# Kernel tuning notes

Hardware: AMD Instinct MI355X
Metric: run time of the kernel (lower is better)

## Reference

```python
import jax, jax.numpy as jnp
import numpy as np

D = 768
NH = 12
HD = D // NH
N_MLP = 3072
LN_EPS = 1e-6


def layer_norm(x, g, b, eps=LN_EPS):
    mu = jnp.mean(x, axis=-1, keepdims=True)
    var = jnp.mean(jnp.square(x - mu), axis=-1, keepdims=True)
    return (x - mu) * jax.lax.rsqrt(var + eps) * g + b


def setup_inputs() -> dict:
    key = jax.random.key(0)
    ks = jax.random.split(key, 6)
    x = jax.random.normal(ks[0], (2, 4096, D), dtype=jnp.float32)
    # torch Linear weights are (out, in); init std=0.02, zero bias
    W_qkv = 0.02 * jax.random.normal(ks[1], (3 * D, D), dtype=jnp.float32)
    b_qkv = jnp.zeros((3 * D,), dtype=jnp.float32)
    W_proj = 0.02 * jax.random.normal(ks[2], (D, D), dtype=jnp.float32)
    b_proj = jnp.zeros((D,), dtype=jnp.float32)
    W1 = 0.02 * jax.random.normal(ks[3], (N_MLP, D), dtype=jnp.float32)
    b1 = jnp.zeros((N_MLP,), dtype=jnp.float32)
    W2 = 0.02 * jax.random.normal(ks[4], (D, N_MLP), dtype=jnp.float32)
    b2 = jnp.zeros((D,), dtype=jnp.float32)
    g1 = jnp.ones((D,), dtype=jnp.float32)
    beta1 = jnp.zeros((D,), dtype=jnp.float32)
    g2 = jnp.ones((D,), dtype=jnp.float32)
    beta2 = jnp.zeros((D,), dtype=jnp.float32)
    return dict(x=x, W_qkv=W_qkv, b_qkv=b_qkv, W_proj=W_proj, b_proj=b_proj,
                W1=W1, b1=b1, W2=W2, b2=b2,
                g1=g1, beta1=beta1, g2=g2, beta2=beta2)


def reference(x, W_qkv, b_qkv, W_proj, b_proj, W1, b1, W2, b2, g1, beta1, g2, beta2):
    B, T, d = x.shape
    scale = HD ** (-0.5)
    # --- attention branch (pre-norm) ---
    h = layer_norm(x, g1, beta1)
    qkv = h @ W_qkv.T + b_qkv                      # [B,T,3d]
    qkv = qkv.reshape(B, T, 3, NH, HD)
    q, k, v = qkv[:, :, 0], qkv[:, :, 1], qkv[:, :, 2]  # [B,T,NH,HD]
    logits = jnp.einsum('bthc,bshc->bhts', q, k) * scale
    attn = jax.nn.softmax(logits, axis=-1)
    out = jnp.einsum('bhts,bshc->bthc', attn, v).reshape(B, T, d)
    out = out @ W_proj.T + b_proj
    x = x + out
    # --- MLP branch (pre-norm) ---
    h = layer_norm(x, g2, beta2)
    h = jax.nn.gelu(h @ W1.T + b1, approximate=False)
    h = h @ W2.T + b2
    return x + h
```

## Files before the change

kernel.cpp:

```cpp
#include <hip/hip_runtime.h>
#include <cmath>

typedef __attribute__((ext_vector_type(4))) float f32x4;
typedef __attribute__((ext_vector_type(16))) float f32x16;
typedef __attribute__((ext_vector_type(8))) __bf16 bf16x8;
typedef __attribute__((ext_vector_type(8))) unsigned short u16x8;
typedef __attribute__((ext_vector_type(4))) unsigned short u16x4;
typedef __attribute__((ext_vector_type(2))) unsigned int u32x2;
typedef __attribute__((ext_vector_type(4))) unsigned int u32x4;

#define DEV __device__ __forceinline__

DEV unsigned short f2b(float v) {
  __bf16 b = (__bf16)v;
  return __builtin_bit_cast(unsigned short, b);
}

DEV unsigned int cvtpk(float lo, float hi) {
  unsigned int r;
  asm("v_cvt_pk_bf16_f32 %0, %1, %2" : "=v"(r) : "v"(lo), "v"(hi));
  return r;
}

DEV float exp2a(float x) {
  float r;
  asm("v_exp_f32 %0, %1" : "=v"(r) : "v"(x));
  return r;
}

DEV void swap32(unsigned int& x, unsigned int& y) {
  asm("v_permlane32_swap_b32 %0, %1" : "+v"(x), "+v"(y));
}

DEV u32x2 tr_b16(const unsigned short* p) {
  u32x2 r;
  asm volatile("ds_read_b64_tr_b16 %0, %1"
               : "=v"(r)
               : "v"((unsigned int)(unsigned long long)p)
               : "memory");
  return r;
}

DEV void gll16(const void* g, const void* l) {
  __builtin_amdgcn_global_load_lds(
      (const __attribute__((address_space(1))) unsigned int*)(unsigned long long)g,
      (__attribute__((address_space(3))) unsigned int*)(unsigned int)(unsigned long long)l,
      16, 0, 0);
}

__global__ void k_cvt_bf16(const float* __restrict__ src,
                           unsigned short* __restrict__ dst, int n4) {
  int i = blockIdx.x * blockDim.x + threadIdx.x;
  if (i >= n4) return;
  float4 v = ((const float4*)src)[i];
  u16x4 o = {f2b(v.x), f2b(v.y), f2b(v.z), f2b(v.w)};
  *(u16x4*)(dst + (size_t)i * 4) = o;
}

__global__ void k_ln(const float* __restrict__ x, const float* __restrict__ g,
                     const float* __restrict__ be, unsigned short* __restrict__ out) {
  int row = blockIdx.x;
  int l = threadIdx.x;
  const float* xr = x + (size_t)row * 768;
  float4 v[3];
  float s = 0.f, sq = 0.f;
#pragma unroll
  for (int j = 0; j < 3; ++j) {
    v[j] = ((const float4*)xr)[l + 64 * j];
    s += v[j].x + v[j].y + v[j].z + v[j].w;
    sq += v[j].x * v[j].x + v[j].y * v[j].y + v[j].z * v[j].z + v[j].w * v[j].w;
  }
#pragma unroll
  for (int m = 1; m < 64; m <<= 1) {
    s += __shfl_xor(s, m);
    sq += __shfl_xor(sq, m);
  }
  float mu = s * (1.f / 768.f);
  float var = sq * (1.f / 768.f) - mu * mu;
  float rs = rsqrtf(var + 1e-6f);
  unsigned short* orow = out + (size_t)row * 768;
#pragma unroll
  for (int j = 0; j < 3; ++j) {
    int c4 = l + 64 * j;
    float4 gv = ((const float4*)g)[c4];
    float4 bv = ((const float4*)be)[c4];
    u16x4 o = {f2b((v[j].x - mu) * rs * gv.x + bv.x),
               f2b((v[j].y - mu) * rs * gv.y + bv.y),
               f2b((v[j].z - mu) * rs * gv.z + bv.z),
               f2b((v[j].w - mu) * rs * gv.w + bv.w)};
    *(u16x4*)(orow + c4 * 4) = o;
  }
}

template <int MODE, int BM>
__global__ __launch_bounds__(256, 2) void k_gemm(
    const unsigned short* __restrict__ A, const unsigned short* __restrict__ Bw,
    const float* __restrict__ bias, const float* __restrict__ res,
    void* __restrict__ outp, int N, int K) {
  __shared__ unsigned short As[3][BM * 32];
  __shared__ unsigned short Bs[3][128 * 32];
  constexpr int MR = BM / 32;
  constexpr int AI = BM / 64;
  constexpr int LPT = AI + 2;
  const int tid = threadIdx.x;
  const int w = tid >> 6, l = tid & 63;
  const int wr = w >> 1, wc = w & 1;
  const int lr = l & 15, lg = l >> 4;
  const int nwg = gridDim.x * gridDim.y;
  const int bid = blockIdx.y * gridDim.x + blockIdx.x;
  const int swz = (bid & 7) * (nwg >> 3) + (bid >> 3);
  const int bx = swz % gridDim.x, by = swz / gridDim.x;
  const int brow = by * BM, bcol = bx * 128;

  auto stage = [&](int buf, int kt) {
#pragma unroll
    for (int i = 0; i < AI; ++i) {
      int c = i * 256 + tid;
      int row = c >> 2, cg = (c & 3) ^ (row & 3);
      gll16(A + (size_t)(brow + row) * K + kt + cg * 8,
            (const char*)&As[buf][0] + (i * 256 + (w << 6)) * 16);
    }
#pragma unroll
    for (int i = 0; i < 2; ++i) {
      int c = i * 256 + tid;
      int row = c >> 2, cg = (c & 3) ^ (row & 3);
      gll16(Bw + (size_t)(bcol + row) * K + kt + cg * 8,
            (const char*)&Bs[buf][0] + (i * 256 + (w << 6)) * 16);
    }
  };

  stage(0, 0);
  if (32 < K) stage(1, 32);
  f32x4 acc[MR][4] = {};
  int cur = 0, nxt2 = 2;
  for (int kt = 0; kt < K; kt += 32) {
    if (kt + 32 < K) {
      if constexpr (LPT == 4)
        asm volatile("s_waitcnt vmcnt(4)" ::: "memory");
      else
        asm volatile("s_waitcnt vmcnt(3)" ::: "memory");
    } else {
      asm volatile("s_waitcnt vmcnt(0)" ::: "memory");
    }
    __builtin_amdgcn_s_barrier();
    __builtin_amdgcn_sched_barrier(0);
    if (kt + 64 < K) {
      stage(nxt2, kt + 64);
      nxt2 = (nxt2 == 2) ? 0 : nxt2 + 1;
    }
    bf16x8 af[MR], bfr[4];
#pragma unroll
    for (int m = 0; m < MR; ++m) {
      int row = wr * (BM / 2) + m * 16 + lr;
      af[m] = *(const bf16x8*)&As[cur][row * 32 + ((lg ^ (row & 3)) << 3)];
    }
#pragma unroll
    for (int n = 0; n < 4; ++n) {
      int row = wc * 64 + n * 16 + lr;
      bfr[n] = *(const bf16x8*)&Bs[cur][row * 32 + ((lg ^ (row & 3)) << 3)];
    }
#pragma unroll
    for (int m = 0; m < MR; ++m)
#pragma unroll
      for (int n = 0; n < 4; ++n)
        acc[m][n] = __builtin_amdgcn_mfma_f32_16x16x32_bf16(af[m], bfr[n], acc[m][n], 0, 0, 0);
    cur = (cur == 2) ? 0 : cur + 1;
  }
#pragma unroll
  for (int n = 0; n < 4; ++n) {
    int col = bcol + wc * 64 + n * 16 + lr;
    float bv = bias[col];
#pragma unroll
    for (int m = 0; m < MR; ++m) {
      int row0 = brow + wr * (BM / 2) + m * 16 + lg * 4;
#pragma unroll
      for (int r = 0; r < 4; ++r) {
        size_t idx = (size_t)(row0 + r) * N + col;
        float v = acc[m][n][r] + bv;
        if (MODE == 0) {
          ((unsigned short*)outp)[idx] = f2b(v);
        } else if (MODE == 1) {
          ((float*)outp)[idx] = v + res[idx];
        } else if (MODE == 2) {
          ((unsigned short*)outp)[idx] = f2b(0.5f * v * (1.f + erff(v * 0.70710678f)));
        } else {
          ((float*)outp)[idx] = v + res[idx];
        }
      }
    }
  }
}

__global__ __launch_bounds__(256, 4) void k_attn(const unsigned short* __restrict__ qkv,
                                                 f32x4* __restrict__ Opart,
                                                 float* __restrict__ ml) {
  __shared__ unsigned short Ks[2][64 * 64];
  __shared__ unsigned short Vs[2][4 * 64 * 16];
  const int tid = threadIdx.x;
  const int w = tid >> 6, l = tid & 63;
  const int lq = l & 31, hi = l >> 5;
  const int p = blockIdx.x;
  const int linear = (p & 7) * 192 + (p >> 3);
  const int bh = linear >> 6, rem = linear & 63;
  const int qt = rem >> 1, half = rem & 1;
  const int b = bh / 12, h = bh % 12;
  const size_t base = (size_t)b * 4096 * 2304;
  const int qbase = qt * 128 + w * 32;
  const int kv0 = half * 2048;

  const float SC = 0.18033688f;
  bf16x8 qb[4];
#pragma unroll
  for (int s = 0; s < 4; ++s) {
    u16x8 raw = *(const u16x8*)(qkv + base + (size_t)(qbase + lq) * 2304 + h * 64 +
                                s * 16 + hi * 8);
    u32x4 pk;
#pragma unroll
    for (int d = 0; d < 4; ++d) {
      float f0 = __builtin_bit_cast(float, (unsigned int)raw[2 * d] << 16) * SC;
      float f1 = __builtin_bit_cast(float, (unsigned int)raw[2 * d + 1] << 16) * SC;
      pk[d] = cvtpk(f0, f1);
    }
    qb[s] = __builtin_bit_cast(bf16x8, pk);
  }

  const unsigned short* pK = qkv + base + (size_t)(kv0 + 16 * w + (l >> 3)) * 2304 + 768 +
                             h * 64 + (((l & 7) ^ ((l >> 3) & 7)) << 3);
  const unsigned short* pV = qkv + base + (size_t)(kv0 + (l >> 1)) * 2304 + 1536 + h * 64 +
                             w * 16 + ((l & 1) << 3);
  const size_t STEP = (size_t)64 * 2304;

  {
    const char* dK = (const char*)&Ks[0][0] + w * 2048;
    const char* dV = (const char*)&Vs[0][0] + w * 2048;
    gll16(pK, dK);
    gll16(pK + 8 * 2304, dK + 1024);
    gll16(pV, dV);
    gll16(pV + 32 * 2304, dV + 1024);
    pK += STEP;
    pV += STEP;
  }

  f32x16 O[2] = {};
  float lrun = 0.f;

  int it = 0;
  for (int t = 0; t < 32; ++t, it ^= 1) {
    asm volatile("s_waitcnt vmcnt(0)" ::: "memory");
    __syncthreads();
    if (t < 31) {
      const char* dK = (const char*)&Ks[it ^ 1][0] + w * 2048;
      const char* dV = (const char*)&Vs[it ^ 1][0] + w * 2048;
      gll16(pK, dK);
      gll16(pK + 8 * 2304, dK + 1024);
      gll16(pV, dV);
      gll16(pV + 32 * 2304, dV + 1024);
      pK += STEP;
      pV += STEP;
    }

    f32x16 st[2] = {{0}, {0}};
    __builtin_amdgcn_s_setprio(1);
#pragma unroll
    for (int kt = 0; kt < 2; ++kt) {
      int key = kt * 32 + lq;
#pragma unroll
      for (int s = 0; s < 4; ++s) {
        bf16x8 ka =
            *(const bf16x8*)&Ks[it][key * 64 + ((s * 16 + hi * 8) ^ ((key & 7) << 3))];
        st[kt] = __builtin_amdgcn_mfma_f32_32x32x16_bf16(ka, qb[s], st[kt], 0, 0, 0);
      }
    }
    __builtin_amdgcn_s_setprio(0);

    float s0 = 0.f, s1 = 0.f, s2 = 0.f, s3 = 0.f;
#pragma unroll
    for (int kt = 0; kt < 2; ++kt) {
#pragma unroll
      for (int r = 0; r < 16; r += 4) {
        float p0 = exp2a(st[kt][r + 0]);
        float p1 = exp2a(st[kt][r + 1]);
        float p2 = exp2a(st[kt][r + 2]);
        float p3 = exp2a(st[kt][r + 3]);
        st[kt][r + 0] = p0;
        st[kt][r + 1] = p1;
        st[kt][r + 2] = p2;
        st[kt][r + 3] = p3;
        s0 += p0;
        s1 += p1;
        s2 += p2;
        s3 += p3;
      }
    }
    float ssum = (s0 + s1) + (s2 + s3);
    lrun += ssum + __shfl_xor(ssum, 32);

    u32x4 pf[4];
#pragma unroll
    for (int kt = 0; kt < 2; ++kt)
#pragma unroll
      for (int h2 = 0; h2 < 2; ++h2) {
        int r0 = h2 * 8;
        unsigned int a0 = cvtpk(st[kt][r0 + 0], st[kt][r0 + 1]);
        unsigned int a1 = cvtpk(st[kt][r0 + 2], st[kt][r0 + 3]);
        unsigned int b0 = cvtpk(st[kt][r0 + 4], st[kt][r0 + 5]);
        unsigned int b1 = cvtpk(st[kt][r0 + 6], st[kt][r0 + 7]);
        swap32(a0, b0);
        swap32(a1, b1);
        pf[kt * 2 + h2] = u32x4{a0, a1, b0, b1};
      }

#pragma unroll
    for (int hb = 0; hb < 2; ++hb) {
      u32x2 vt[4][2];
      const unsigned short* vbase = &Vs[it][(hb * 2 + (lq >> 4)) * 1024 + (lq & 15)];
#pragma unroll
      for (int s = 0; s < 4; ++s)
#pragma unroll
        for (int t2 = 0; t2 < 2; ++t2)
          vt[s][t2] = tr_b16(vbase + ((s * 16 + hi * 8 + t2 * 4) << 4));
      asm volatile("s_waitcnt lgkmcnt(0)" ::: "memory");
      __builtin_amdgcn_sched_barrier(0);
      __builtin_amdgcn_s_setprio(1);
#pragma unroll
      for (int s = 0; s < 4; ++s) {
        u32x4 vv = {vt[s][0].x, vt[s][0].y, vt[s][1].x, vt[s][1].y};
        O[hb] = __builtin_amdgcn_mfma_f32_32x32x16_bf16(
            __builtin_bit_cast(bf16x8, vv), __builtin_bit_cast(bf16x8, pf[s]), O[hb], 0, 0, 0);
      }
      __builtin_amdgcn_s_setprio(0);
    }
  }

  if (hi == 0) ml[(linear * 4 + w) * 32 + lq] = lrun;
#pragma unroll
  for (int hb = 0; hb < 2; ++hb)
#pragma unroll
    for (int g = 0; g < 4; ++g) {
      int k = hb * 4 + g;
      f32x4 v = {O[hb][4 * g + 0], O[hb][4 * g + 1], O[hb][4 * g + 2], O[hb][4 * g + 3]};
      Opart[((linear * 4 + w) * 8 + k) * 64 + l] = v;
    }
}

__global__ __launch_bounds__(256) void k_merge(const f32x4* __restrict__ Opart,
                                               const float* __restrict__ ml,
                                               unsigned short* __restrict__ out) {
  const int g = blockIdx.x;
  const int bh = g >> 5, qt = g & 31;
  const int b = bh / 12, h = bh % 12;
  const int tid = threadIdx.x;
  const int w = tid >> 6, l = tid & 63;
  const int lq = l & 31, hi = l >> 5;
  const int bidA = bh * 64 + qt * 2;
  const int bidB = bidA + 1;
  float l0 = ml[(bidA * 4 + w) * 32 + lq];
  float l1 = ml[(bidB * 4 + w) * 32 + lq];
  float rl = 1.f / (l0 + l1);
  const int t = qt * 128 + w * 32 + lq;
  unsigned short* orow = out + (size_t)(b * 4096 + t) * 768 + h * 64;
#pragma unroll
  for (int hb = 0; hb < 2; ++hb)
#pragma unroll
    for (int gg = 0; gg < 4; ++gg) {
      int k = hb * 4 + gg;
      f32x4 va = Opart[((bidA * 4 + w) * 8 + k) * 64 + l];
      f32x4 vb = Opart[((bidB * 4 + w) * 8 + k) * 64 + l];
      f32x4 v = (va + vb) * rl;
      unsigned int d0 = cvtpk(v[0], v[1]);
      unsigned int d1 = cvtpk(v[2], v[3]);
      *(u32x2*)(orow + hb * 32 + 8 * gg + 4 * hi) = u32x2{d0, d1};
    }
}

extern "C" void kernel_launch(void* const* d_in, const int* in_sizes, int n_in,
                              void* d_out, int out_size, void* d_ws, size_t ws_size,
                              hipStream_t stream) {
  const float* x = (const float*)d_in[0];
  const float* Wqkv = (const float*)d_in[1];
  const float* bqkv = (const float*)d_in[2];
  const float* Wproj = (const float*)d_in[3];
  const float* bproj = (const float*)d_in[4];
  const float* W1 = (const float*)d_in[5];
  const float* b1 = (const float*)d_in[6];
  const float* W2 = (const float*)d_in[7];
  const float* b2 = (const float*)d_in[8];
  const float* g1 = (const float*)d_in[9];
  const float* be1 = (const float*)d_in[10];
  const float* g2 = (const float*)d_in[11];
  const float* be2 = (const float*)d_in[12];

  char* ws = (char*)d_ws;
  unsigned short* wqkv = (unsigned short*)(ws + 0);
  unsigned short* wproj = (unsigned short*)(ws + 3538944);
  unsigned short* ww1 = (unsigned short*)(ws + 4718592);
  unsigned short* ww2 = (unsigned short*)(ws + 9437184);
  unsigned short* h1 = (unsigned short*)(ws + 14155776);
  unsigned short* qkvb = (unsigned short*)(ws + 26738688);
  unsigned short* attno = (unsigned short*)(ws + 64487424);
  float* x1 = (float*)(ws + 77070336);
  unsigned short* h2 = (unsigned short*)(ws + 102236160);
  unsigned short* m1 = (unsigned short*)(ws + 114819072);
  f32x4* Opart = (f32x4*)m1;
  float* mlbuf = (float*)h1;

  k_cvt_bf16<<<1728, 256, 0, stream>>>(Wqkv, wqkv, 442368);
  k_cvt_bf16<<<576, 256, 0, stream>>>(Wproj, wproj, 147456);
  k_cvt_bf16<<<2304, 256, 0, stream>>>(W1, ww1, 589824);
  k_cvt_bf16<<<2304, 256, 0, stream>>>(W2, ww2, 589824);

  k_ln<<<8192, 64, 0, stream>>>(x, g1, be1, h1);
  k_gemm<0, 128><<<dim3(18, 64), 256, 0, stream>>>(h1, wqkv, bqkv, nullptr, qkvb, 2304, 768);
  k_attn<<<1536, 256, 0, stream>>>(qkvb, Opart, mlbuf);
  k_merge<<<768, 256, 0, stream>>>(Opart, mlbuf, attno);
  k_gemm<1, 64><<<dim3(6, 128), 256, 0, stream>>>(attno, wproj, bproj, x, x1, 768, 768);
  k_ln<<<8192, 64, 0, stream>>>(x1, g2, be2, h2);
  k_gemm<2, 128><<<dim3(24, 64), 256, 0, stream>>>(h2, ww1, b1, nullptr, m1, 3072, 768);
  k_gemm<3, 64><<<dim3(6, 128), 256, 0, stream>>>(m1, ww2, b2, x1, (float*)d_out, 768, 3072);
}
```

Baseline: 356.2 us.

## Use BK=64 double-buffered GEMM pipeline and store attention partials in bf16

The GEMM now stages 64-wide K tiles into two LDS buffers instead of 32-wide tiles into three, using an 8-way XOR swizzle. Each tile's fragments are read into registers, then a second barrier lets the next load into the same buffer start during the MFMA burst, which runs at raised priority. This halves the barrier count per K and doubles the MFMA work per iteration, at the cost of more LDS and registers. Separately, the split-KV attention partial outputs are packed to bf16 before writing and unpacked in the merge kernel, halving that intermediate traffic at some precision cost.

```diff
diff --git a/kernel.cpp b/kernel.cpp
--- a/kernel.cpp
+++ b/kernel.cpp
@@ -47,6 +47,9 @@
       (__attribute__((address_space(3))) unsigned int*)(unsigned int)(unsigned long long)l,
       16, 0, 0);
 }
+
+DEV float bflo(unsigned int u) { return __builtin_bit_cast(float, u << 16); }
+DEV float bfhi(unsigned int u) { return __builtin_bit_cast(float, u & 0xFFFF0000u); }
 
 __global__ void k_cvt_bf16(const float* __restrict__ src,
                            unsigned short* __restrict__ dst, int n4) {
@@ -97,11 +100,11 @@
     const unsigned short* __restrict__ A, const unsigned short* __restrict__ Bw,
     const float* __restrict__ bias, const float* __restrict__ res,
     void* __restrict__ outp, int N, int K) {
-  __shared__ unsigned short As[3][BM * 32];
-  __shared__ unsigned short Bs[3][128 * 32];
+  __shared__ unsigned short As[2][BM * 64];
+  __shared__ unsigned short Bs[2][128 * 64];
   constexpr int MR = BM / 32;
-  constexpr int AI = BM / 64;
-  constexpr int LPT = AI + 2;
+  constexpr int AI = BM / 32;
+  constexpr int LPT = AI + 4;
   const int tid = threadIdx.x;
   const int w = tid >> 6, l = tid & 63;
   const int wr = w >> 1, wc = w & 1;
@@ -116,55 +119,63 @@
 #pragma unroll
     for (int i = 0; i < AI; ++i) {
       int c = i * 256 + tid;
-      int row = c >> 2, cg = (c & 3) ^ (row & 3);
+      int row = c >> 3, cg = (c & 7) ^ (row & 7);
       gll16(A + (size_t)(brow + row) * K + kt + cg * 8,
             (const char*)&As[buf][0] + (i * 256 + (w << 6)) * 16);
     }
 #pragma unroll
-    for (int i = 0; i < 2; ++i) {
+    for (int i = 0; i < 4; ++i) {
       int c = i * 256 + tid;
-      int row = c >> 2, cg = (c & 3) ^ (row & 3);
+      int row = c >> 3, cg = (c & 7) ^ (row & 7);
       gll16(Bw + (size_t)(bcol + row) * K + kt + cg * 8,
             (const char*)&Bs[buf][0] + (i * 256 + (w << 6)) * 16);
     }
   };
 
   stage(0, 0);
-  if (32 < K) stage(1, 32);
+  if (64 < K) stage(1, 64);
   f32x4 acc[MR][4] = {};
-  int cur = 0, nxt2 = 2;
-  for (int kt = 0; kt < K; kt += 32) {
-    if (kt + 32 < K) {
-      if constexpr (LPT == 4)
-        asm volatile("s_waitcnt vmcnt(4)" ::: "memory");
+  for (int kt = 0, t = 0; kt < K; kt += 64, ++t) {
+    const int cur = t & 1;
+    if (kt + 64 < K) {
+      if constexpr (LPT == 8)
+        asm volatile("s_waitcnt vmcnt(8)" ::: "memory");
       else
-        asm volatile("s_waitcnt vmcnt(3)" ::: "memory");
+        asm volatile("s_waitcnt vmcnt(6)" ::: "memory");
     } else {
       asm volatile("s_waitcnt vmcnt(0)" ::: "memory");
     }
     __builtin_amdgcn_s_barrier();
     __builtin_amdgcn_sched_barrier(0);
-    if (kt + 64 < K) {
-      stage(nxt2, kt + 64);
-      nxt2 = (nxt2 == 2) ? 0 : nxt2 + 1;
-    }
-    bf16x8 af[MR], bfr[4];
+    bf16x8 af[MR][2], bfr[4][2];
 #pragma unroll
     for (int m = 0; m < MR; ++m) {
       int row = wr * (BM / 2) + m * 16 + lr;
-      af[m] = *(const bf16x8*)&As[cur][row * 32 + ((lg ^ (row & 3)) << 3)];
+#pragma unroll
+      for (int s = 0; s < 2; ++s)
+        af[m][s] = *(const bf16x8*)&As[cur][row * 64 + (((s * 4 + lg) ^ (row & 7)) << 3)];
     }
 #pragma unroll
     for (int n = 0; n < 4; ++n) {
       int row = wc * 64 + n * 16 + lr;
-      bfr[n] = *(const bf16x8*)&Bs[cur][row * 32 + ((lg ^ (row & 3)) << 3)];
-    }
-#pragma unroll
-    for (int m = 0; m < MR; ++m)
-#pragma unroll
-      for (int n = 0; n < 4; ++n)
-        acc[m][n] = __builtin_amdgcn_mfma_f32_16x16x32_bf16(af[m], bfr[n], acc[m][n], 0, 0, 0);
-    cur = (cur == 2) ? 0 : cur + 1;
+#pragma unroll
+      for (int s = 0; s < 2; ++s)
+        bfr[n][s] = *(const bf16x8*)&Bs[cur][row * 64 + (((s * 4 + lg) ^ (row & 7)) << 3)];
+    }
+    asm volatile("s_waitcnt lgkmcnt(0)" ::: "memory");
+    __builtin_amdgcn_sched_barrier(0);
+    __builtin_amdgcn_s_barrier();
+    if (kt + 128 < K) stage(cur, kt + 128);
+    __builtin_amdgcn_s_setprio(1);
+#pragma unroll
+    for (int s = 0; s < 2; ++s)
+#pragma unroll
+      for (int m = 0; m < MR; ++m)
+#pragma unroll
+        for (int n = 0; n < 4; ++n)
+          acc[m][n] =
+              __builtin_amdgcn_mfma_f32_16x16x32_bf16(af[m][s], bfr[n][s], acc[m][n], 0, 0, 0);
+    __builtin_amdgcn_s_setprio(0);
   }
 #pragma unroll
   for (int n = 0; n < 4; ++n) {
@@ -192,7 +203,7 @@
 }
 
 __global__ __launch_bounds__(256, 4) void k_attn(const unsigned short* __restrict__ qkv,
-                                                 f32x4* __restrict__ Opart,
+                                                 u32x4* __restrict__ Opk,
                                                  float* __restrict__ ml) {
   __shared__ unsigned short Ks[2][64 * 64];
   __shared__ unsigned short Vs[2][4 * 64 * 16];
@@ -336,14 +347,16 @@
 #pragma unroll
   for (int hb = 0; hb < 2; ++hb)
 #pragma unroll
-    for (int g = 0; g < 4; ++g) {
-      int k = hb * 4 + g;
-      f32x4 v = {O[hb][4 * g + 0], O[hb][4 * g + 1], O[hb][4 * g + 2], O[hb][4 * g + 3]};
-      Opart[((linear * 4 + w) * 8 + k) * 64 + l] = v;
-    }
-}
-
-__global__ __launch_bounds__(256) void k_merge(const f32x4* __restrict__ Opart,
+    for (int v = 0; v < 2; ++v) {
+      u32x4 pkv = {cvtpk(O[hb][8 * v + 0], O[hb][8 * v + 1]),
+                   cvtpk(O[hb][8 * v + 2], O[hb][8 * v + 3]),
+                   cvtpk(O[hb][8 * v + 4], O[hb][8 * v + 5]),
+                   cvtpk(O[hb][8 * v + 6], O[hb][8 * v + 7])};
+      Opk[((linear * 4 + w) * 4 + hb * 2 + v) * 64 + l] = pkv;
+    }
+}
+
+__global__ __launch_bounds__(256) void k_merge(const u32x4* __restrict__ Opk,
                                                const float* __restrict__ ml,
                                                unsigned short* __restrict__ out) {
   const int g = blockIdx.x;
@@ -362,14 +375,18 @@
 #pragma unroll
   for (int hb = 0; hb < 2; ++hb)
 #pragma unroll
-    for (int gg = 0; gg < 4; ++gg) {
-      int k = hb * 4 + gg;
-      f32x4 va = Opart[((bidA * 4 + w) * 8 + k) * 64 + l];
-      f32x4 vb = Opart[((bidB * 4 + w) * 8 + k) * 64 + l];
-      f32x4 v = (va + vb) * rl;
-      unsigned int d0 = cvtpk(v[0], v[1]);
-      unsigned int d1 = cvtpk(v[2], v[3]);
-      *(u32x2*)(orow + hb * 32 + 8 * gg + 4 * hi) = u32x2{d0, d1};
+    for (int v = 0; v < 2; ++v) {
+      u32x4 va = Opk[((bidA * 4 + w) * 4 + hb * 2 + v) * 64 + l];
+      u32x4 vb = Opk[((bidB * 4 + w) * 4 + hb * 2 + v) * 64 + l];
+      unsigned int dw[4];
+#pragma unroll
+      for (int d = 0; d < 4; ++d) {
+        float lo = (bflo(va[d]) + bflo(vb[d])) * rl;
+        float hi2 = (bfhi(va[d]) + bfhi(vb[d])) * rl;
+        dw[d] = cvtpk(lo, hi2);
+      }
+      *(u32x2*)(orow + hb * 32 + 8 * (2 * v) + 4 * hi) = u32x2{dw[0], dw[1]};
+      *(u32x2*)(orow + hb * 32 + 8 * (2 * v + 1) + 4 * hi) = u32x2{dw[2], dw[3]};
     }
 }
 
@@ -401,7 +418,7 @@
   float* x1 = (float*)(ws + 77070336);
   unsigned short* h2 = (unsigned short*)(ws + 102236160);
   unsigned short* m1 = (unsigned short*)(ws + 114819072);
-  f32x4* Opart = (f32x4*)m1;
+  u32x4* Opk = (u32x4*)m1;
   float* mlbuf = (float*)h1;
 
   k_cvt_bf16<<<1728, 256, 0, stream>>>(Wqkv, wqkv, 442368);
@@ -411,8 +428,8 @@
 
   k_ln<<<8192, 64, 0, stream>>>(x, g1, be1, h1);
   k_gemm<0, 128><<<dim3(18, 64), 256, 0, stream>>>(h1, wqkv, bqkv, nullptr, qkvb, 2304, 768);
-  k_attn<<<1536, 256, 0, stream>>>(qkvb, Opart, mlbuf);
-  k_merge<<<768, 256, 0, stream>>>(Opart, mlbuf, attno);
+  k_attn<<<1536, 256, 0, stream>>>(qkvb, Opk, mlbuf);
+  k_merge<<<768, 256, 0, stream>>>(Opk, mlbuf, attno);
   k_gemm<1, 64><<<dim3(6, 128), 256, 0, stream>>>(attno, wproj, bproj, x, x1, 768, 768);
   k_ln<<<8192, 64, 0, stream>>>(x1, g2, be2, h2);
   k_gemm<2, 128><<<dim3(24, 64), 256, 0, stream>>>(h2, ww1, b1, nullptr, m1, 3072, 768);
```

New measurement: 345.1 us. 1.03x faster.
